# Performance work log

Hardware: AMD Instinct MI355X
Metric: run time of the kernel (lower is better)

Reference implementation:

```python
import jax, jax.numpy as jnp
import numpy as np

RADIUS = 3
TEMP = 0.1
EPS = 1e-6


def bilinear_resize(x, oh, ow):
    # Matches torch F.interpolate(mode='bilinear', align_corners=False):
    # half-pixel centers, source coord clamped to >= 0, no antialiasing.
    b, c, h, w = x.shape
    ys = jnp.maximum((jnp.arange(oh, dtype=x.dtype) + 0.5) * (h / oh) - 0.5, 0.0)
    xs = jnp.maximum((jnp.arange(ow, dtype=x.dtype) + 0.5) * (w / ow) - 0.5, 0.0)
    y0f = jnp.floor(ys)
    x0f = jnp.floor(xs)
    wy = (ys - y0f)[:, None]          # [oh,1]
    wx = (xs - x0f)[None, :]          # [1,ow]
    y0 = jnp.clip(y0f, 0, h - 1).astype(jnp.int32)
    y1 = jnp.clip(y0f + 1, 0, h - 1).astype(jnp.int32)
    x0 = jnp.clip(x0f, 0, w - 1).astype(jnp.int32)
    x1 = jnp.clip(x0f + 1, 0, w - 1).astype(jnp.int32)
    r0 = x[:, :, y0, :]
    r1 = x[:, :, y1, :]
    v00 = r0[:, :, :, x0]; v01 = r0[:, :, :, x1]
    v10 = r1[:, :, :, x0]; v11 = r1[:, :, :, x1]
    return (1 - wy) * ((1 - wx) * v00 + wx * v01) + wy * ((1 - wx) * v10 + wx * v11)


def setup_inputs() -> dict:
    key = jax.random.key(0)
    k1, k2, k3 = jax.random.split(key, 3)
    fL = jax.random.normal(k1, (4, 256, 96, 320), dtype=jnp.float32)
    fR = jax.random.normal(k2, (4, 256, 96, 320), dtype=jnp.float32)
    disp_full = jax.random.uniform(k3, (4, 1, 384, 1280), dtype=jnp.float32) * 64.0
    return {"fL": fL, "fR": fR, "disp_full": disp_full}


def reference(fL, fR, disp_full):
    B, C, h4, w4 = fL.shape
    H, W = disp_full.shape[-2], disp_full.shape[-1]
    # quarter-res disparity
    disp0 = bilinear_resize(disp_full, h4, w4) / 4.0            # [B,1,h4,w4]
    # cosine correlation volume over 2*radius+1 horizontal shifts
    nL = fL / jnp.clip(jnp.linalg.norm(fL, axis=1, keepdims=True), EPS)
    nR = fR / jnp.clip(jnp.linalg.norm(fR, axis=1, keepdims=True), EPS)
    sims = [jnp.sum(nL * jnp.roll(nR, d, axis=-1), axis=1)
            for d in range(-RADIUS, RADIUS + 1)]
    # original wraps build_cosine_cost in @torch.no_grad()
    cost = jax.lax.stop_gradient(jnp.stack(sims, axis=1))       # [B,7,h4,w4]
    p = jax.nn.softmax(cost / TEMP, axis=1)
    offsets = jnp.arange(-RADIUS, RADIUS + 1, dtype=fL.dtype).reshape(1, -1, 1, 1)
    delta = jnp.sum(p * offsets, axis=1, keepdims=True)          # [B,1,h4,w4]
    disp_ref = disp0 + delta
    conf = jnp.max(p, axis=1, keepdims=True)
    # laplacian smoothing (smooth=True)
    lap = jnp.array([[0., 1., 0.], [1., -4., 1.], [0., 1., 0.]], dtype=fL.dtype).reshape(1, 1, 3, 3)
    lap_out = jax.lax.conv_general_dilated(disp_ref, lap, (1, 1), [(1, 1), (1, 1)])
    disp_q = disp_ref - 0.2 * lap_out
    disp_full_ref = bilinear_resize(disp_q, H, W) * 4.0
    conf_full = bilinear_resize(conf, H, W)
    return disp_full_ref, conf_full
```

## Files before the change

kernel.cpp:

```cpp
#include <hip/hip_runtime.h>
#include <math.h>

constexpr int B_ = 4, C_ = 256, H4 = 96, W4 = 320, HF = 384, WF = 1280;
constexpr int CHUNKS = 5;
constexpr float EPSV = 1e-6f;
constexpr int LOW = B_ * H4 * W4;
constexpr int FULL = B_ * HF * WF;

__global__ __launch_bounds__(256)
void phase1(const float* __restrict__ fL, const float* __restrict__ fR,
            const float* __restrict__ D, float* __restrict__ dref,
            float* __restrict__ conf)
{
    const int bi = blockIdx.x;
    const int chunk = bi % CHUNKS;
    const int y = (bi / CHUNKS) % H4;
    const int b = bi / (CHUNKS * H4);
    const int tid = threadIdx.x;
    const int wave = tid >> 6;
    const int lane = tid & 63;
    const int x0 = chunk * 64;
    const int x = x0 + lane;

    const size_t chanStride = (size_t)H4 * W4;
    const size_t rowBase = (((size_t)b * C_) * H4 + y) * W4;

    int hx = 0, hslot = 0;
    const bool isHalo = (lane < 6);
    if (lane < 3)      { hx = x0 - 3 + lane;        if (hx < 0)   hx += W4; hslot = lane; }
    else if (lane < 6) { hx = x0 + 64 + (lane - 3); if (hx >= W4) hx -= W4; hslot = 64 + lane; }

    float dot[7] = {0.f,0.f,0.f,0.f,0.f,0.f,0.f};
    float ssL = 0.f, ssR = 0.f, ssH = 0.f;

    __shared__ float stage[4][72];
    float* const sw = stage[wave];

    const float* pLx = fL + rowBase + (size_t)(wave * 64) * chanStride + x;
    const float* pRx = fR + rowBase + (size_t)(wave * 64) * chanStride + x;
    const float* pRh = fR + rowBase + (size_t)(wave * 64) * chanStride + hx;

#pragma unroll 4
    for (int c = 0; c < 64; ++c) {
        const float a  = *pLx;
        const float rv = *pRx;
        sw[3 + lane] = rv;
        if (isHalo) {
            const float h = *pRh;
            sw[hslot] = h;
            ssH += h * h;
        }
        __asm__ volatile("s_waitcnt lgkmcnt(0)" ::: "memory");
        float r[7];
#pragma unroll
        for (int k = 0; k < 7; ++k) r[k] = sw[lane + k];
        ssL += a * a;
        ssR += rv * rv;
#pragma unroll
        for (int k = 0; k < 7; ++k) dot[k] += a * r[k];
        pLx += chanStride; pRx += chanStride; pRh += chanStride;
    }

    __shared__ float part[256][11];
    __shared__ float sss[70];
#pragma unroll
    for (int k = 0; k < 7; ++k) part[tid][k] = dot[k];
    part[tid][7] = ssL;
    part[tid][8] = ssR;
    part[tid][9] = ssH;
    __syncthreads();

    float rdot[7], rssL = 0.f;
    if (tid < 64) {
#pragma unroll
        for (int k = 0; k < 7; ++k)
            rdot[k] = part[tid][k] + part[tid + 64][k] + part[tid + 128][k] + part[tid + 192][k];
        rssL = part[tid][7] + part[tid + 64][7] + part[tid + 128][7] + part[tid + 192][7];
        float rssR = part[tid][8] + part[tid + 64][8] + part[tid + 128][8] + part[tid + 192][8];
        sss[3 + tid] = rssR;
        if (tid < 6) {
            float hh = part[tid][9] + part[tid + 64][9] + part[tid + 128][9] + part[tid + 192][9];
            if (tid < 3) sss[tid] = hh;
            else         sss[64 + tid] = hh;
        }
    }
    __syncthreads();

    if (tid < 64) {
        const float nL = fmaxf(sqrtf(rssL), EPSV);
        float cost[7];
#pragma unroll
        for (int k = 0; k < 7; ++k) {
            float nR = fmaxf(sqrtf(sss[tid + k]), EPSV);
            float s = rdot[k] / (nL * nR);
            cost[6 - k] = s * 10.0f;
        }
        float m = cost[0];
#pragma unroll
        for (int i = 1; i < 7; ++i) m = fmaxf(m, cost[i]);
        float sum = 0.f, dsum = 0.f;
#pragma unroll
        for (int i = 0; i < 7; ++i) {
            float e = __expf(cost[i] - m);
            sum += e;
            dsum += e * (float)(i - 3);
        }
        const float delta = dsum / sum;
        const float cf = 1.0f / sum;

        const int xpix = x0 + tid;
        const int Y0 = 4 * y + 1, X0 = 4 * xpix + 1;
        const size_t dbase = ((size_t)b * HF + Y0) * WF + X0;
        const float s4 = D[dbase] + D[dbase + 1] + D[dbase + WF] + D[dbase + WF + 1];
        const float disp0 = s4 * 0.0625f;

        const size_t o = ((size_t)b * H4 + y) * W4 + xpix;
        dref[o] = disp0 + delta;
        conf[o] = cf;
    }
}

__device__ __forceinline__ float dq_val(const float* __restrict__ dref,
                                        size_t base, int yq, int xq)
{
    size_t i = base + (size_t)yq * W4 + xq;
    float c  = dref[i];
    float up = (yq > 0)      ? dref[i - W4] : 0.f;
    float dn = (yq < H4 - 1) ? dref[i + W4] : 0.f;
    float lf = (xq > 0)      ? dref[i - 1]  : 0.f;
    float rt = (xq < W4 - 1) ? dref[i + 1]  : 0.f;
    return c - 0.2f * (up + dn + lf + rt - 4.f * c);
}

__global__ void phase2(const float* __restrict__ dref, const float* __restrict__ cf,
                       float* __restrict__ out)
{
    int i = blockIdx.x * blockDim.x + threadIdx.x;
    if (i >= FULL) return;
    int X = i % WF;
    int Y = (i / WF) % HF;
    int b = i / (WF * HF);
    float ys = fmaxf((Y + 0.5f) * 0.25f - 0.5f, 0.f);
    float xs = fmaxf((X + 0.5f) * 0.25f - 0.5f, 0.f);
    float y0f = floorf(ys), x0f = floorf(xs);
    float wy = ys - y0f, wx = xs - x0f;
    int y0 = min((int)y0f, H4 - 1);
    int x0 = min((int)x0f, W4 - 1);
    int y1 = min(y0 + 1, H4 - 1);
    int x1 = min(x0 + 1, W4 - 1);
    size_t base = (size_t)b * (H4 * W4);

    float d = (1.f - wy) * ((1.f - wx) * dq_val(dref, base, y0, x0) + wx * dq_val(dref, base, y0, x1))
            +        wy  * ((1.f - wx) * dq_val(dref, base, y1, x0) + wx * dq_val(dref, base, y1, x1));

    size_t i00 = base + (size_t)y0 * W4 + x0;
    size_t i01 = base + (size_t)y0 * W4 + x1;
    size_t i10 = base + (size_t)y1 * W4 + x0;
    size_t i11 = base + (size_t)y1 * W4 + x1;
    float cv = (1.f - wy) * ((1.f - wx) * cf[i00] + wx * cf[i01])
             +        wy  * ((1.f - wx) * cf[i10] + wx * cf[i11]);

    out[i] = 4.0f * d;
    out[(size_t)FULL + i] = cv;
}

extern "C" void kernel_launch(void* const* d_in, const int* in_sizes, int n_in,
                              void* d_out, int out_size, void* d_ws, size_t ws_size,
                              hipStream_t stream)
{
    const float* fL = (const float*)d_in[0];
    const float* fR = (const float*)d_in[1];
    const float* D  = (const float*)d_in[2];
    float* out  = (float*)d_out;
    float* ws   = (float*)d_ws;
    float* dref = ws;
    float* conf = ws + LOW;

    phase1<<<B_ * H4 * CHUNKS, 256, 0, stream>>>(fL, fR, D, dref, conf);
    phase2<<<(FULL + 255) / 256, 256, 0, stream>>>(dref, conf, out);
}
```

Before: 289.7 us.

## Batch four channels per LDS exchange and prefetch next channel group

The channel loop now handles four channels per iteration, packing the right-feature values into float4 LDS entries. This cuts the number of LDS store/wait/load rounds by four and widens each LDS access. The global loads for the next four channels are issued before the LDS wait, using a waitcnt that only waits on LDS, so memory latency overlaps the dot-product work. Every lane now loads a halo value (hx defaults to x), which adds redundant global loads, and the extra prefetch registers may lower occupancy.

```diff
diff --git a/kernel.cpp b/kernel.cpp
--- a/kernel.cpp
+++ b/kernel.cpp
@@ -25,7 +25,7 @@
     const size_t chanStride = (size_t)H4 * W4;
     const size_t rowBase = (((size_t)b * C_) * H4 + y) * W4;
 
-    int hx = 0, hslot = 0;
+    int hx = x, hslot = 0;
     const bool isHalo = (lane < 6);
     if (lane < 3)      { hx = x0 - 3 + lane;        if (hx < 0)   hx += W4; hslot = lane; }
     else if (lane < 6) { hx = x0 + 64 + (lane - 3); if (hx >= W4) hx -= W4; hslot = 64 + lane; }
@@ -33,32 +33,47 @@
     float dot[7] = {0.f,0.f,0.f,0.f,0.f,0.f,0.f};
     float ssL = 0.f, ssR = 0.f, ssH = 0.f;
 
-    __shared__ float stage[4][72];
-    float* const sw = stage[wave];
+    __shared__ float4 stage4[4][72];
+    float4* const sw = stage4[wave];
 
-    const float* pLx = fL + rowBase + (size_t)(wave * 64) * chanStride + x;
-    const float* pRx = fR + rowBase + (size_t)(wave * 64) * chanStride + x;
-    const float* pRh = fR + rowBase + (size_t)(wave * 64) * chanStride + hx;
+    const float* pLb = fL + rowBase + (size_t)(wave * 64) * chanStride;
+    const float* pRb = fR + rowBase + (size_t)(wave * 64) * chanStride;
+
+    float aa[4], rr[4], hh[4];
+    size_t off = 0;
+#pragma unroll
+    for (int j = 0; j < 4; ++j) {
+        aa[j] = pLb[off + x]; rr[j] = pRb[off + x]; hh[j] = pRb[off + hx];
+        off += chanStride;
+    }
 
 #pragma unroll 4
-    for (int c = 0; c < 64; ++c) {
-        const float a  = *pLx;
-        const float rv = *pRx;
-        sw[3 + lane] = rv;
-        if (isHalo) {
-            const float h = *pRh;
-            sw[hslot] = h;
-            ssH += h * h;
+    for (int it = 0; it < 16; ++it) {
+        const float ca0 = aa[0], ca1 = aa[1], ca2 = aa[2], ca3 = aa[3];
+        const float4 rq = make_float4(rr[0], rr[1], rr[2], rr[3]);
+        const float4 hq = make_float4(hh[0], hh[1], hh[2], hh[3]);
+
+        sw[3 + lane] = rq;
+        if (isHalo) sw[hslot] = hq;
+
+        if (it < 15) {
+#pragma unroll
+            for (int j = 0; j < 4; ++j) {
+                aa[j] = pLb[off + x]; rr[j] = pRb[off + x]; hh[j] = pRb[off + hx];
+                off += chanStride;
+            }
         }
-        __asm__ volatile("s_waitcnt lgkmcnt(0)" ::: "memory");
-        float r[7];
+
+        __builtin_amdgcn_s_waitcnt(0xC07F);
+
 #pragma unroll
-        for (int k = 0; k < 7; ++k) r[k] = sw[lane + k];
-        ssL += a * a;
-        ssR += rv * rv;
-#pragma unroll
-        for (int k = 0; k < 7; ++k) dot[k] += a * r[k];
-        pLx += chanStride; pRx += chanStride; pRh += chanStride;
+        for (int k = 0; k < 7; ++k) {
+            const float4 t = sw[lane + k];
+            dot[k] += ca0 * t.x + ca1 * t.y + ca2 * t.z + ca3 * t.w;
+        }
+        ssL += ca0 * ca0 + ca1 * ca1 + ca2 * ca2 + ca3 * ca3;
+        ssR += rq.x * rq.x + rq.y * rq.y + rq.z * rq.z + rq.w * rq.w;
+        ssH += hq.x * hq.x + hq.y * hq.y + hq.z * hq.z + hq.w * hq.w;
     }
 
     __shared__ float part[256][11];
@@ -79,9 +94,9 @@
         float rssR = part[tid][8] + part[tid + 64][8] + part[tid + 128][8] + part[tid + 192][8];
         sss[3 + tid] = rssR;
         if (tid < 6) {
-            float hh = part[tid][9] + part[tid + 64][9] + part[tid + 128][9] + part[tid + 192][9];
-            if (tid < 3) sss[tid] = hh;
-            else         sss[64 + tid] = hh;
+            float hh2 = part[tid][9] + part[tid + 64][9] + part[tid + 128][9] + part[tid + 192][9];
+            if (tid < 3) sss[tid] = hh2;
+            else         sss[64 + tid] = hh2;
         }
     }
     __syncthreads();
```

Result: no change. 286.8 us (-1.0%).
